# Optimization experiments

Hardware: AMD Instinct MI355X
Metric: run time of the kernel (lower is better)

The kernel has to match this reference:

```python
import jax, jax.numpy as jnp
import numpy as np

B, N, M, C1, C2 = 16, 4096, 1024, 128, 256
MLP0, MLP1 = 256, 256
IN_CH = C1 + C2
EPS = 1e-5


def setup_inputs() -> dict:
    key = jax.random.key(0)
    ks = jax.random.split(key, 6)
    return {
        "xyz1": jax.random.normal(ks[0], (B, 3, N), jnp.float32),
        "xyz2": jax.random.normal(ks[1], (B, 3, M), jnp.float32),
        "points1": jax.random.normal(ks[2], (B, C1, N), jnp.float32),
        "points2": jax.random.normal(ks[3], (B, C2, M), jnp.float32),
        "W1": jax.random.normal(ks[4], (MLP0, IN_CH), jnp.float32) * (1.0 / np.sqrt(IN_CH)),
        "gamma1": jnp.ones((MLP0,), jnp.float32),
        "beta1": jnp.zeros((MLP0,), jnp.float32),
        "W2": jax.random.normal(ks[5], (MLP1, MLP0), jnp.float32) * (1.0 / np.sqrt(MLP0)),
        "gamma2": jnp.ones((MLP1,), jnp.float32),
        "beta2": jnp.zeros((MLP1,), jnp.float32),
    }


def _batchnorm(x, gamma, beta):
    # x: (B, N, C); normalize per channel over batch*length (training-mode BN, biased var)
    mean = jnp.mean(x, axis=(0, 1))
    var = jnp.mean((x - mean) ** 2, axis=(0, 1))
    return (x - mean) * jax.lax.rsqrt(var + EPS) * gamma + beta


def reference(xyz1, xyz2, points1, points2, W1, gamma1, beta1, W2, gamma2, beta2):
    p1 = jnp.swapaxes(xyz1, 1, 2)  # (B, N, 3)
    p2 = jnp.swapaxes(xyz2, 1, 2)  # (B, M, 3)
    # squared pairwise distances (B, N, M); squaring preserves 3-NN ordering,
    # and the original squares the euclidean dist before weighting anyway
    d2 = jnp.sum((p1[:, :, None, :] - p2[:, None, :, :]) ** 2, axis=-1)
    neg_d2, idx = jax.lax.top_k(-d2, 3)  # 3 smallest distances
    dist2 = jnp.maximum(-neg_d2, 1e-10)  # (B, N, 3)
    inv = 1.0 / dist2
    weight = inv / jnp.sum(inv, axis=-1, keepdims=True)  # (B, N, 3)
    f2 = jnp.swapaxes(points2, 1, 2)  # (B, M, C2)
    b, n, k = idx.shape
    gathered = jnp.take_along_axis(
        f2, idx.reshape(b, n * k)[:, :, None], axis=1
    ).reshape(b, n, k, -1)  # (B, N, 3, C2)
    interp = jnp.einsum("bnk,bnkc->bnc", weight, gathered)  # (B, N, C2)
    feat = jnp.concatenate([interp, jnp.swapaxes(points1, 1, 2)], axis=-1)  # (B, N, C1+C2)
    h = jnp.einsum("bnc,oc->bno", feat, W1)  # conv1d k=1, no bias
    h = jax.nn.relu(_batchnorm(h, gamma1, beta1))
    h = jnp.einsum("bnc,oc->bno", h, W2)
    h = jax.nn.relu(_batchnorm(h, gamma2, beta2))
    return jnp.swapaxes(h, 1, 2)  # (B, MLP1, N), channel-first like torch
```

## Files before the change

kernel.cpp:

```cpp
#include <hip/hip_runtime.h>

typedef unsigned short u16;
typedef unsigned int u32;

#define BB 16
#define NN 4096
#define MM 1024
#define C1V 128
#define C2V 256
#define O1 256
#define O2 256
#define EPSV 1e-5f
#define INV_CNT (1.0f/65536.0f)
#define NREP 32

typedef __attribute__((ext_vector_type(8))) short bf16x8;
typedef __attribute__((ext_vector_type(4))) float f32x4;

static __device__ __forceinline__ u16 f2b(float f) {
  u32 u = __float_as_uint(f);
  u32 r = (u + 0x7FFFu + ((u >> 16) & 1u)) >> 16;
  return (u16)r;
}
static __device__ __forceinline__ float b2f(u16 s) {
  return __uint_as_float(((u32)s) << 16);
}

#define GLD_LDS16(gp, lp)                                                      \
  __builtin_amdgcn_global_load_lds(                                            \
      (const __attribute__((address_space(1))) void*)(gp),                     \
      (__attribute__((address_space(3))) void*)(lp), 16, 0, 0)

__global__ __launch_bounds__(256) void knn_kernel(
    const float* __restrict__ xyz1, const float* __restrict__ xyz2,
    float* __restrict__ pd, int* __restrict__ pi) {
  __shared__ float4 cand[256];
  int bx = blockIdx.x;
  int c = bx & 3;
  int qt = (bx >> 2) & 7;
  int b = bx >> 5;
  int t = threadIdx.x;

  const float* x2b = xyz2 + b * 3 * MM;
  {
    float x = x2b[c * 256 + t];
    float y = x2b[MM + c * 256 + t];
    float z = x2b[2 * MM + c * 256 + t];
    cand[t] = make_float4(x, y, z, x * x + y * y + z * z);
  }
  __syncthreads();

  const float* x1b = xyz1 + b * 3 * NN;
  int n0 = qt * 512 + t;
  int n1 = n0 + 256;
  float px0 = x1b[n0], py0 = x1b[NN + n0], pz0 = x1b[2 * NN + n0];
  float px1 = x1b[n1], py1 = x1b[NN + n1], pz1 = x1b[2 * NN + n1];

  const float INF = 3.4e38f;
  float k00 = INF, k01 = INF, k02 = INF;
  float k10 = INF, k11 = INF, k12 = INF;
  int j00 = 0, j01 = 0, j02 = 0;
  int j10 = 0, j11 = 0, j12 = 0;

#pragma unroll 8
  for (int m = 0; m < 256; ++m) {
    float4 cd = cand[m];
    {
      float dot = fmaf(px0, cd.x, fmaf(py0, cd.y, pz0 * cd.z));
      float key = fmaf(-2.0f, dot, cd.w);
      bool c0 = key < k00, c1 = key < k01, c2 = key < k02;
      k02 = c1 ? k01 : (c2 ? key : k02);
      j02 = c1 ? j01 : (c2 ? m : j02);
      k01 = c0 ? k00 : (c1 ? key : k01);
      j01 = c0 ? j00 : (c1 ? m : j01);
      k00 = c0 ? key : k00;
      j00 = c0 ? m : j00;
    }
    {
      float dot = fmaf(px1, cd.x, fmaf(py1, cd.y, pz1 * cd.z));
      float key = fmaf(-2.0f, dot, cd.w);
      bool c0 = key < k10, c1 = key < k11, c2 = key < k12;
      k12 = c1 ? k11 : (c2 ? key : k12);
      j12 = c1 ? j11 : (c2 ? m : j12);
      k11 = c0 ? k10 : (c1 ? key : k11);
      j11 = c0 ? j10 : (c1 ? m : j11);
      k10 = c0 ? key : k10;
      j10 = c0 ? m : j10;
    }
  }

  float pn0 = px0 * px0 + py0 * py0 + pz0 * pz0;
  float pn1 = px1 * px1 + py1 * py1 + pz1 * pz1;
  int gq0 = b * NN + n0;
  int gq1 = b * NN + n1;
  int base = c << 8;
  ((float4*)pd)[(size_t)c * 65536 + gq0] =
      make_float4(fmaxf(k00 + pn0, 1e-10f), fmaxf(k01 + pn0, 1e-10f),
                  fmaxf(k02 + pn0, 1e-10f), 0.0f);
  ((int4*)pi)[(size_t)c * 65536 + gq0] =
      make_int4(base + j00, base + j01, base + j02, 0);
  ((float4*)pd)[(size_t)c * 65536 + gq1] =
      make_float4(fmaxf(k10 + pn1, 1e-10f), fmaxf(k11 + pn1, 1e-10f),
                  fmaxf(k12 + pn1, 1e-10f), 0.0f);
  ((int4*)pi)[(size_t)c * 65536 + gq1] =
      make_int4(base + j10, base + j11, base + j12, 0);
}

__global__ __launch_bounds__(256) void cast_w_kernel(
    const float* __restrict__ W1, const float* __restrict__ W2,
    u16* __restrict__ d1, u16* __restrict__ d2) {
  int i = blockIdx.x * 256 + threadIdx.x;
  if (i < 98304) d1[i] = f2b(W1[i]);
  else if (i < 163840) d2[i - 98304] = f2b(W2[i - 98304]);
}

__global__ __launch_bounds__(256) void tcast_kernel(
    const float* __restrict__ in, u16* __restrict__ out, int C, int P) {
  __shared__ float tile[32][33];
  int tx = threadIdx.x & 31, ty = threadIdx.x >> 5;
  int p0 = blockIdx.x * 32, c0 = blockIdx.y * 32, b = blockIdx.z;
  const float* ib = in + (size_t)b * C * P;
  u16* ob = out + (size_t)b * P * C;
#pragma unroll
  for (int i = 0; i < 4; ++i)
    tile[ty + i * 8][tx] = ib[(size_t)(c0 + ty + i * 8) * P + p0 + tx];
  __syncthreads();
#pragma unroll
  for (int i = 0; i < 4; ++i)
    ob[(size_t)(p0 + ty + i * 8) * C + c0 + tx] = f2b(tile[tx][ty + i * 8]);
}

template <int K, int NTILES, bool INTERP, bool STATS, bool OUTB, bool BNA>
__global__ __launch_bounds__(256) void gemm_mfma(
    const u16* __restrict__ A, int lda, const u16* __restrict__ B, int ldb,
    void* __restrict__ out, const u16* __restrict__ G,
    const float* __restrict__ pd, const int* __restrict__ pi,
    float* __restrict__ statsOut, const float* __restrict__ statsInR,
    const float* __restrict__ gamma, const float* __restrict__ beta) {
  __shared__ u16 smem[16384];
  __shared__ float wsh[128][3];
  __shared__ int ish[128][3];
  __shared__ float scA[256], shA[256];

  int t = threadIdx.x;
  int w = t >> 6, l = t & 63;
  int n0;
  if (NTILES > 0) {
    int p = blockIdx.x;
    int batch = ((p & 7) << 1) | ((p >> 3) & 1);
    int nt = p >> 4;
    n0 = (batch * NTILES + nt) * 128;
  } else {
    n0 = blockIdx.x * 128;
  }
  int o0 = blockIdx.y * 128;

  if (INTERP) {
    if (t < 128) {
      int gq = n0 + t;
      float4 d0 = ((const float4*)pd)[gq];
      int4 ii0 = ((const int4*)pi)[gq];
      float a0 = d0.x, a1 = d0.y, a2 = d0.z;
      int b0 = ii0.x, b1 = ii0.y, b2 = ii0.z;
#pragma unroll
      for (int c = 1; c < 4; ++c) {
        float4 dc = ((const float4*)pd)[(size_t)c * 65536 + gq];
        int4 ic = ((const int4*)pi)[(size_t)c * 65536 + gq];
        float kv[3] = {dc.x, dc.y, dc.z};
        int jv[3] = {ic.x, ic.y, ic.z};
#pragma unroll
        for (int j = 0; j < 3; ++j) {
          float key = kv[j];
          int idx = jv[j];
          bool c0 = key < a0, c1 = key < a1, c2 = key < a2;
          a2 = c1 ? a1 : (c2 ? key : a2);
          b2 = c1 ? b1 : (c2 ? idx : b2);
          a1 = c0 ? a0 : (c1 ? key : a1);
          b1 = c0 ? b0 : (c1 ? idx : b1);
          a0 = c0 ? key : a0;
          b0 = c0 ? idx : b0;
        }
      }
      float v0 = 1.0f / a0, v1 = 1.0f / a1, v2 = 1.0f / a2;
      float s = 1.0f / (v0 + v1 + v2);
      wsh[t][0] = v0 * s; wsh[t][1] = v1 * s; wsh[t][2] = v2 * s;
      ish[t][0] = b0;     ish[t][1] = b1;     ish[t][2] = b2;
    }
  }
  if (BNA) {
    float s = 0.0f, qq = 0.0f;
#pragma unroll
    for (int r = 0; r < NREP; ++r) {
      s += statsInR[r * 512 + t];
      qq += statsInR[r * 512 + 256 + t];
    }
    float mean = s * INV_CNT;
    float var = qq * INV_CNT - mean * mean;
    float sc = rsqrtf(var + EPSV) * gamma[t];
    scA[t] = sc;
    shA[t] = beta[t] - mean * sc;
  }

  int wm = w & 1, wn = w >> 1;
  int lr = l >> 2, lc = l & 3;
  int q = l >> 4, m = l & 15;

  f32x4 acc[4][4] = {};
  u16* As = smem;
  u16* Bs = smem + 4096;

  const u16* arow = A + (size_t)n0 * lda;
  const u16* brow = B + (size_t)o0 * ldb;

#pragma unroll
  for (int kt = 0; kt < K; kt += 32) {
    __syncthreads();
#pragma unroll
    for (int r = 0; r < 2; ++r) {
      int row = r * 64 + w * 16 + lr;
      if (BNA) {
        union { uint4 u; u16 s[8]; } v, o;
        v.u = *(const uint4*)(arow + (size_t)row * lda + kt + lc * 8);
        int cb = kt + lc * 8;
#pragma unroll
        for (int j = 0; j < 8; ++j) {
          float f = fmaf(b2f(v.s[j]), scA[cb + j], shA[cb + j]);
          o.s[j] = f2b(fmaxf(f, 0.0f));
        }
        *(uint4*)(As + row * 32 + lc * 8) = o.u;
      } else {
        GLD_LDS16(arow + (size_t)row * lda + kt + lc * 8, As + row * 32 + lc * 8);
      }
    }
#pragma unroll
    for (int r = 0; r < 2; ++r) {
      int row = r * 64 + w * 16 + lr;
      GLD_LDS16(brow + (size_t)row * ldb + kt + lc * 8, Bs + row * 32 + lc * 8);
    }
    __syncthreads();
    bf16x8 af[4], bf[4];
#pragma unroll
    for (int i = 0; i < 4; ++i)
      af[i] = *(const bf16x8*)(As + (wm * 64 + i * 16 + m) * 32 + q * 8);
#pragma unroll
    for (int j = 0; j < 4; ++j)
      bf[j] = *(const bf16x8*)(Bs + (wn * 64 + j * 16 + m) * 32 + q * 8);
#pragma unroll
    for (int i = 0; i < 4; ++i)
#pragma unroll
      for (int j = 0; j < 4; ++j)
        acc[i][j] =
            __builtin_amdgcn_mfma_f32_16x16x32_bf16(af[i], bf[j], acc[i][j], 0, 0, 0);
  }

  if (INTERP) {
    __syncthreads();
    int b = n0 >> 12;
    int rl = t >> 1, half = t & 1, rx = rl & 7;
    float w0 = wsh[rl][0], w1 = wsh[rl][1], w2 = wsh[rl][2];
    const u16* g0 = G + ((size_t)(b * 1024 + ish[rl][0])) * 256 + o0 + half * 64;
    const u16* g1 = G + ((size_t)(b * 1024 + ish[rl][1])) * 256 + o0 + half * 64;
    const u16* g2 = G + ((size_t)(b * 1024 + ish[rl][2])) * 256 + o0 + half * 64;
#pragma unroll
    for (int c8 = 0; c8 < 8; ++c8) {
      bf16x8 v0 = *(const bf16x8*)(g0 + c8 * 8);
      bf16x8 v1 = *(const bf16x8*)(g1 + c8 * 8);
      bf16x8 v2 = *(const bf16x8*)(g2 + c8 * 8);
      union { uint4 u; u16 s[8]; } o;
#pragma unroll
      for (int e = 0; e < 8; ++e) {
        float f = w0 * b2f((u16)v0[e]) + w1 * b2f((u16)v1[e]) +
                  w2 * b2f((u16)v2[e]);
        o.s[e] = f2b(f);
      }
      int ch = (half * 8 + c8) ^ rx;
      *(uint4*)(smem + rl * 128 + ch * 8) = o.u;
    }
    __syncthreads();
#pragma unroll
    for (int i = 0; i < 4; ++i)
#pragma unroll
      for (int reg = 0; reg < 4; ++reg) {
        int row = wm * 64 + i * 16 + q * 4 + reg;
        int rxr = row & 7;
#pragma unroll
        for (int j = 0; j < 4; ++j) {
          int col = wn * 64 + j * 16 + m;
          int off = row * 128 + (((col >> 3) ^ rxr) << 3) + (col & 7);
          acc[i][j][reg] += b2f(smem[off]);
        }
      }
  }

  if (STATS) {
    int rep = blockIdx.x & (NREP - 1);
#pragma unroll
    for (int j = 0; j < 4; ++j) {
      float s = 0.0f, ss = 0.0f;
#pragma unroll
      for (int i = 0; i < 4; ++i)
#pragma unroll
        for (int reg = 0; reg < 4; ++reg) {
          float v = acc[i][j][reg];
          s += v;
          ss += v * v;
        }
      s += __shfl_down(s, 32); ss += __shfl_down(ss, 32);
      s += __shfl_down(s, 16); ss += __shfl_down(ss, 16);
      if (l < 16) {
        int c = o0 + wn * 64 + j * 16 + l;
        atomicAdd(&statsOut[rep * 512 + c], s);
        atomicAdd(&statsOut[rep * 512 + 256 + c], ss);
      }
    }
  }

#pragma unroll
  for (int i = 0; i < 4; ++i) {
    int gr = n0 + wm * 64 + i * 16 + q * 4;
#pragma unroll
    for (int reg = 0; reg < 4; ++reg) {
#pragma unroll
      for (int j = 0; j < 4; ++j) {
        int gc = o0 + wn * 64 + j * 16 + m;
        size_t off = (size_t)(gr + reg) * 256 + gc;
        if (OUTB)
          ((u16*)out)[off] = f2b(acc[i][j][reg]);
        else
          ((float*)out)[off] = acc[i][j][reg];
      }
    }
  }
}

__global__ __launch_bounds__(256) void bn2t_kernel(
    const u16* __restrict__ h2, const float* __restrict__ statsR,
    const float* __restrict__ gamma, const float* __restrict__ beta,
    float* __restrict__ out) {
  __shared__ float tile[32][33];
  __shared__ float sS[32], sH[32];
  int t = threadIdx.x;
  int tx = t & 31, ty = t >> 5;
  int n0 = blockIdx.x * 32, c0 = blockIdx.y * 32, b = blockIdx.z;
  if (t < 32) {
    int c = c0 + t;
    float s = 0.0f, qq = 0.0f;
#pragma unroll
    for (int r = 0; r < NREP; ++r) {
      s += statsR[r * 512 + c];
      qq += statsR[r * 512 + 256 + c];
    }
    float mean = s * INV_CNT;
    float var = qq * INV_CNT - mean * mean;
    float sc = rsqrtf(var + EPSV) * gamma[c];
    sS[t] = sc;
    sH[t] = beta[c] - mean * sc;
  }
  __syncthreads();
#pragma unroll
  for (int i = 0; i < 4; ++i) {
    int n = n0 + ty + i * 8;
    float v = b2f(h2[((size_t)b * NN + n) * 256 + c0 + tx]) * sS[tx] + sH[tx];
    tile[ty + i * 8][tx] = fmaxf(v, 0.0f);
  }
  __syncthreads();
#pragma unroll
  for (int i = 0; i < 4; ++i)
    out[((size_t)b * 256 + c0 + ty + i * 8) * NN + n0 + tx] = tile[tx][ty + i * 8];
}

extern "C" void kernel_launch(void* const* d_in, const int* in_sizes, int n_in,
                              void* d_out, int out_size, void* d_ws,
                              size_t ws_size, hipStream_t stream) {
  const float* xyz1    = (const float*)d_in[0];
  const float* xyz2    = (const float*)d_in[1];
  const float* points1 = (const float*)d_in[2];
  const float* points2 = (const float*)d_in[3];
  const float* W1      = (const float*)d_in[4];
  const float* gamma1  = (const float*)d_in[5];
  const float* beta1   = (const float*)d_in[6];
  const float* W2      = (const float*)d_in[7];
  const float* gamma2  = (const float*)d_in[8];
  const float* beta2   = (const float*)d_in[9];

  char* ws = (char*)d_ws;
  float* stats1R = (float*)(ws + 0);
  float* stats2R = (float*)(ws + 65536);
  u16*   W1b     = (u16*)(ws + 131072);
  u16*   W2b     = (u16*)(ws + 327680);
  u16*   p2t     = (u16*)(ws + 458752);
  u16*   p1t     = (u16*)(ws + 8847360);
  u16*   G       = (u16*)(ws + 25624576);
  u16*   h2b     = (u16*)(ws + 34013184);
  float* pd      = (float*)(ws + 67567616);
  int*   pi      = (int*)(ws + 71761920);
  u16*   h1b     = (u16*)d_out;
  float* out     = (float*)d_out;

  hipMemsetAsync(stats1R, 0, 131072, stream);
  knn_kernel<<<512, 256, 0, stream>>>(xyz1, xyz2, pd, pi);
  cast_w_kernel<<<640, 256, 0, stream>>>(W1, W2, W1b, W2b);
  tcast_kernel<<<dim3(32, 8, 16), 256, 0, stream>>>(points2, p2t, C2V, MM);
  tcast_kernel<<<dim3(128, 4, 16), 256, 0, stream>>>(points1, p1t, C1V, NN);
  gemm_mfma<256, 8, false, false, true, false><<<dim3(128, 2), 256, 0, stream>>>(
      p2t, 256, W1b, 384, G, nullptr, nullptr, nullptr, nullptr, nullptr,
      nullptr, nullptr);
  gemm_mfma<128, 32, true, true, true, false><<<dim3(512, 2), 256, 0, stream>>>(
      p1t, 128, W1b + 256, 384, h1b, G, pd, pi, stats1R, nullptr, nullptr,
      nullptr);
  gemm_mfma<256, 0, false, true, true, true><<<dim3(512, 2), 256, 0, stream>>>(
      h1b, 256, W2b, 256, h2b, nullptr, nullptr, nullptr, stats2R, stats1R,
      gamma1, beta1);
  bn2t_kernel<<<dim3(128, 8, 16), 256, 0, stream>>>(h2b, stats2R, gamma2,
                                                    beta2, out);
}
```

Measured before the change: 251.3 us.

## Merge prep kernels into one launch and stage bf16 GEMM output through LDS

Replaces the memset, knn, weight-cast and two transpose-cast launches with a single block-partitioned prep kernel, so launch gaps go away and the small independent jobs can run concurrently. The bf16 GEMM epilogue now writes accumulators into shared memory and then stores coalesced 16-byte rows instead of scattered 2-byte stores. The cost is a larger, heterogeneous kernel whose shared-memory and register needs are set by the knn branch, plus two extra barriers in the epilogue.

```diff
diff --git a/kernel.cpp b/kernel.cpp
--- a/kernel.cpp
+++ b/kernel.cpp
@@ -31,94 +31,11 @@
       (const __attribute__((address_space(1))) void*)(gp),                     \
       (__attribute__((address_space(3))) void*)(lp), 16, 0, 0)
 
-__global__ __launch_bounds__(256) void knn_kernel(
-    const float* __restrict__ xyz1, const float* __restrict__ xyz2,
-    float* __restrict__ pd, int* __restrict__ pi) {
-  __shared__ float4 cand[256];
-  int bx = blockIdx.x;
-  int c = bx & 3;
-  int qt = (bx >> 2) & 7;
-  int b = bx >> 5;
-  int t = threadIdx.x;
-
-  const float* x2b = xyz2 + b * 3 * MM;
-  {
-    float x = x2b[c * 256 + t];
-    float y = x2b[MM + c * 256 + t];
-    float z = x2b[2 * MM + c * 256 + t];
-    cand[t] = make_float4(x, y, z, x * x + y * y + z * z);
-  }
-  __syncthreads();
-
-  const float* x1b = xyz1 + b * 3 * NN;
-  int n0 = qt * 512 + t;
-  int n1 = n0 + 256;
-  float px0 = x1b[n0], py0 = x1b[NN + n0], pz0 = x1b[2 * NN + n0];
-  float px1 = x1b[n1], py1 = x1b[NN + n1], pz1 = x1b[2 * NN + n1];
-
-  const float INF = 3.4e38f;
-  float k00 = INF, k01 = INF, k02 = INF;
-  float k10 = INF, k11 = INF, k12 = INF;
-  int j00 = 0, j01 = 0, j02 = 0;
-  int j10 = 0, j11 = 0, j12 = 0;
-
-#pragma unroll 8
-  for (int m = 0; m < 256; ++m) {
-    float4 cd = cand[m];
-    {
-      float dot = fmaf(px0, cd.x, fmaf(py0, cd.y, pz0 * cd.z));
-      float key = fmaf(-2.0f, dot, cd.w);
-      bool c0 = key < k00, c1 = key < k01, c2 = key < k02;
-      k02 = c1 ? k01 : (c2 ? key : k02);
-      j02 = c1 ? j01 : (c2 ? m : j02);
-      k01 = c0 ? k00 : (c1 ? key : k01);
-      j01 = c0 ? j00 : (c1 ? m : j01);
-      k00 = c0 ? key : k00;
-      j00 = c0 ? m : j00;
-    }
-    {
-      float dot = fmaf(px1, cd.x, fmaf(py1, cd.y, pz1 * cd.z));
-      float key = fmaf(-2.0f, dot, cd.w);
-      bool c0 = key < k10, c1 = key < k11, c2 = key < k12;
-      k12 = c1 ? k11 : (c2 ? key : k12);
-      j12 = c1 ? j11 : (c2 ? m : j12);
-      k11 = c0 ? k10 : (c1 ? key : k11);
-      j11 = c0 ? j10 : (c1 ? m : j11);
-      k10 = c0 ? key : k10;
-      j10 = c0 ? m : j10;
-    }
-  }
-
-  float pn0 = px0 * px0 + py0 * py0 + pz0 * pz0;
-  float pn1 = px1 * px1 + py1 * py1 + pz1 * pz1;
-  int gq0 = b * NN + n0;
-  int gq1 = b * NN + n1;
-  int base = c << 8;
-  ((float4*)pd)[(size_t)c * 65536 + gq0] =
-      make_float4(fmaxf(k00 + pn0, 1e-10f), fmaxf(k01 + pn0, 1e-10f),
-                  fmaxf(k02 + pn0, 1e-10f), 0.0f);
-  ((int4*)pi)[(size_t)c * 65536 + gq0] =
-      make_int4(base + j00, base + j01, base + j02, 0);
-  ((float4*)pd)[(size_t)c * 65536 + gq1] =
-      make_float4(fmaxf(k10 + pn1, 1e-10f), fmaxf(k11 + pn1, 1e-10f),
-                  fmaxf(k12 + pn1, 1e-10f), 0.0f);
-  ((int4*)pi)[(size_t)c * 65536 + gq1] =
-      make_int4(base + j10, base + j11, base + j12, 0);
-}
-
-__global__ __launch_bounds__(256) void cast_w_kernel(
-    const float* __restrict__ W1, const float* __restrict__ W2,
-    u16* __restrict__ d1, u16* __restrict__ d2) {
-  int i = blockIdx.x * 256 + threadIdx.x;
-  if (i < 98304) d1[i] = f2b(W1[i]);
-  else if (i < 163840) d2[i - 98304] = f2b(W2[i - 98304]);
-}
-
-__global__ __launch_bounds__(256) void tcast_kernel(
-    const float* __restrict__ in, u16* __restrict__ out, int C, int P) {
-  __shared__ float tile[32][33];
+__device__ __forceinline__ void tcast_tile(const float* __restrict__ in,
+                                           u16* __restrict__ out, int C, int P,
+                                           int p0, int c0, int b,
+                                           float (*tile)[33]) {
   int tx = threadIdx.x & 31, ty = threadIdx.x >> 5;
-  int p0 = blockIdx.x * 32, c0 = blockIdx.y * 32, b = blockIdx.z;
   const float* ib = in + (size_t)b * C * P;
   u16* ob = out + (size_t)b * P * C;
 #pragma unroll
@@ -128,6 +45,100 @@
 #pragma unroll
   for (int i = 0; i < 4; ++i)
     ob[(size_t)(p0 + ty + i * 8) * C + c0 + tx] = f2b(tile[tx][ty + i * 8]);
+}
+
+__global__ __launch_bounds__(256) void prep_kernel(
+    const float* __restrict__ xyz1, const float* __restrict__ xyz2,
+    float* __restrict__ pd, int* __restrict__ pi,
+    const float* __restrict__ points1, const float* __restrict__ points2,
+    u16* __restrict__ p1t, u16* __restrict__ p2t,
+    const float* __restrict__ W1, const float* __restrict__ W2,
+    u16* __restrict__ W1b, u16* __restrict__ W2b,
+    float* __restrict__ statsZero) {
+  __shared__ float4 cand[256];
+  __shared__ float tile[32][33];
+  int bx = blockIdx.x;
+  int t = threadIdx.x;
+
+  if (bx < 512) {
+    int c = bx & 3;
+    int qt = (bx >> 2) & 7;
+    int b = bx >> 5;
+    const float* x2b = xyz2 + b * 3 * MM;
+    {
+      float x = x2b[c * 256 + t];
+      float y = x2b[MM + c * 256 + t];
+      float z = x2b[2 * MM + c * 256 + t];
+      cand[t] = make_float4(x, y, z, x * x + y * y + z * z);
+    }
+    __syncthreads();
+    const float* x1b = xyz1 + b * 3 * NN;
+    int n0 = qt * 512 + t;
+    int n1 = n0 + 256;
+    float px0 = x1b[n0], py0 = x1b[NN + n0], pz0 = x1b[2 * NN + n0];
+    float px1 = x1b[n1], py1 = x1b[NN + n1], pz1 = x1b[2 * NN + n1];
+    const float INF = 3.4e38f;
+    float k00 = INF, k01 = INF, k02 = INF;
+    float k10 = INF, k11 = INF, k12 = INF;
+    int j00 = 0, j01 = 0, j02 = 0;
+    int j10 = 0, j11 = 0, j12 = 0;
+#pragma unroll 8
+    for (int m = 0; m < 256; ++m) {
+      float4 cd = cand[m];
+      {
+        float dot = fmaf(px0, cd.x, fmaf(py0, cd.y, pz0 * cd.z));
+        float key = fmaf(-2.0f, dot, cd.w);
+        bool c0 = key < k00, c1 = key < k01, c2 = key < k02;
+        k02 = c1 ? k01 : (c2 ? key : k02);
+        j02 = c1 ? j01 : (c2 ? m : j02);
+        k01 = c0 ? k00 : (c1 ? key : k01);
+        j01 = c0 ? j00 : (c1 ? m : j01);
+        k00 = c0 ? key : k00;
+        j00 = c0 ? m : j00;
+      }
+      {
+        float dot = fmaf(px1, cd.x, fmaf(py1, cd.y, pz1 * cd.z));
+        float key = fmaf(-2.0f, dot, cd.w);
+        bool c0 = key < k10, c1 = key < k11, c2 = key < k12;
+        k12 = c1 ? k11 : (c2 ? key : k12);
+        j12 = c1 ? j11 : (c2 ? m : j12);
+        k11 = c0 ? k10 : (c1 ? key : k11);
+        j11 = c0 ? j10 : (c1 ? m : j11);
+        k10 = c0 ? key : k10;
+        j10 = c0 ? m : j10;
+      }
+    }
+    float pn0 = px0 * px0 + py0 * py0 + pz0 * pz0;
+    float pn1 = px1 * px1 + py1 * py1 + pz1 * pz1;
+    int gq0 = b * NN + n0;
+    int gq1 = b * NN + n1;
+    int base = c << 8;
+    ((float4*)pd)[(size_t)c * 65536 + gq0] =
+        make_float4(fmaxf(k00 + pn0, 1e-10f), fmaxf(k01 + pn0, 1e-10f),
+                    fmaxf(k02 + pn0, 1e-10f), 0.0f);
+    ((int4*)pi)[(size_t)c * 65536 + gq0] =
+        make_int4(base + j00, base + j01, base + j02, 0);
+    ((float4*)pd)[(size_t)c * 65536 + gq1] =
+        make_float4(fmaxf(k10 + pn1, 1e-10f), fmaxf(k11 + pn1, 1e-10f),
+                    fmaxf(k12 + pn1, 1e-10f), 0.0f);
+    ((int4*)pi)[(size_t)c * 65536 + gq1] =
+        make_int4(base + j10, base + j11, base + j12, 0);
+  } else if (bx < 1152) {
+    int i = (bx - 512) * 256 + t;
+    if (i < 98304) W1b[i] = f2b(W1[i]);
+    else if (i < 163840) W2b[i - 98304] = f2b(W2[i - 98304]);
+  } else if (bx < 1184) {
+    ((float4*)statsZero)[(bx - 1152) * 256 + t] =
+        make_float4(0.f, 0.f, 0.f, 0.f);
+  } else if (bx < 5280) {
+    int local = bx - 1184;
+    int pt = local & 31, ct = (local >> 5) & 7, b = local >> 8;
+    tcast_tile(points2, p2t, C2V, MM, pt * 32, ct * 32, b, tile);
+  } else {
+    int local = bx - 5280;
+    int pt = local & 127, ct = (local >> 7) & 3, b = local >> 9;
+    tcast_tile(points1, p1t, C1V, NN, pt * 32, ct * 32, b, tile);
+  }
 }
 
 template <int K, int NTILES, bool INTERP, bool STATS, bool OUTB, bool BNA>
@@ -315,20 +326,38 @@
     }
   }
 
-#pragma unroll
-  for (int i = 0; i < 4; ++i) {
-    int gr = n0 + wm * 64 + i * 16 + q * 4;
-#pragma unroll
-    for (int reg = 0; reg < 4; ++reg) {
-#pragma unroll
-      for (int j = 0; j < 4; ++j) {
-        int gc = o0 + wn * 64 + j * 16 + m;
-        size_t off = (size_t)(gr + reg) * 256 + gc;
-        if (OUTB)
-          ((u16*)out)[off] = f2b(acc[i][j][reg]);
-        else
-          ((float*)out)[off] = acc[i][j][reg];
-      }
+  if (OUTB) {
+    __syncthreads();
+#pragma unroll
+    for (int i = 0; i < 4; ++i)
+#pragma unroll
+      for (int reg = 0; reg < 4; ++reg) {
+        int row = wm * 64 + i * 16 + q * 4 + reg;
+#pragma unroll
+        for (int j = 0; j < 4; ++j)
+          smem[row * 128 + wn * 64 + j * 16 + m] = f2b(acc[i][j][reg]);
+      }
+    __syncthreads();
+    u16* outp = (u16*)out;
+    int rbase = w * 32 + (l >> 4);
+    int seg = l & 15;
+#pragma unroll
+    for (int itr = 0; itr < 8; ++itr) {
+      int row = rbase + itr * 4;
+      uint4 v = *(const uint4*)(smem + row * 128 + seg * 8);
+      *(uint4*)(outp + (size_t)(n0 + row) * 256 + o0 + seg * 8) = v;
+    }
+  } else {
+#pragma unroll
+    for (int i = 0; i < 4; ++i) {
+      int gr = n0 + wm * 64 + i * 16 + q * 4;
+#pragma unroll
+      for (int reg = 0; reg < 4; ++reg)
+#pragma unroll
+        for (int j = 0; j < 4; ++j) {
+          int gc = o0 + wn * 64 + j * 16 + m;
+          ((float*)out)[(size_t)(gr + reg) * 256 + gc] = acc[i][j][reg];
+        }
     }
   }
 }
@@ -397,11 +426,8 @@
   u16*   h1b     = (u16*)d_out;
   float* out     = (float*)d_out;
 
-  hipMemsetAsync(stats1R, 0, 131072, stream);
-  knn_kernel<<<512, 256, 0, stream>>>(xyz1, xyz2, pd, pi);
-  cast_w_kernel<<<640, 256, 0, stream>>>(W1, W2, W1b, W2b);
-  tcast_kernel<<<dim3(32, 8, 16), 256, 0, stream>>>(points2, p2t, C2V, MM);
-  tcast_kernel<<<dim3(128, 4, 16), 256, 0, stream>>>(points1, p1t, C1V, NN);
+  prep_kernel<<<13472, 256, 0, stream>>>(xyz1, xyz2, pd, pi, points1, points2,
+                                         p1t, p2t, W1, W2, W1b, W2b, stats1R);
   gemm_mfma<256, 8, false, false, true, false><<<dim3(128, 2), 256, 0, stream>>>(
       p2t, 256, W1b, 384, G, nullptr, nullptr, nullptr, nullptr, nullptr,
       nullptr, nullptr);
```

After: 233.1 us. 1.08x faster.
